# Kernel tuning notes

Measured on AMD Instinct MI355X. Metric: run time of the kernel, lower is better.

## Reference

```python
import jax, jax.numpy as jnp
import numpy as np

# ---- forest structure (static) ----
B = 32                      # number of trees in the batch
DEPTH = 12                  # topological levels per tree
LEVELS = [2 ** d for d in range(DEPTH)]           # nodes per level (root=level 0)
STARTS = np.concatenate([[0], np.cumsum(LEVELS)[:-1]]).astype(int)
NPG = int(sum(LEVELS))      # 4095 nodes per graph, node 0 = root
N = B * NPG                 # 131040 total nodes
VOCAB = 20000               # dataset.PAD_TOKEN_VALUE + 1
PAD = VOCAB - 1             # padding_idx
E = 256                     # embedding_dim (x_size)
H = 256                     # lstm_output_dim (h_size)
C = 104                     # num_classes (extra_non_linear=None)


def setup_inputs() -> dict:
    key = jax.random.key(0)
    ks = jax.random.split(key, 8)
    # random parent in the previous level for every non-root node (irregular fan-in)
    rng = np.random.RandomState(0)
    par = np.full(N, -1, dtype=np.int64)
    for g in range(B):
        off = g * NPG
        for d in range(1, DEPTH):
            nd = LEVELS[d]
            par[off + STARTS[d]: off + STARTS[d] + nd] = (
                off + STARTS[d - 1] + rng.randint(0, LEVELS[d - 1], size=nd))
    s = 0.05
    return {
        'x': jax.random.randint(ks[0], (N,), 0, VOCAB),
        'par': jnp.asarray(par),
        'emb': jax.random.normal(ks[1], (VOCAB, E), jnp.float32) * s,
        'W_iou': jax.random.normal(ks[2], (3 * H, E), jnp.float32) * s,
        'U_iou': jax.random.normal(ks[3], (3 * H, H), jnp.float32) * s,
        'b_iou': jnp.zeros((1, 3 * H), jnp.float32),
        'U_f_w': jax.random.normal(ks[4], (H, H), jnp.float32) * s,
        'U_f_b': jnp.zeros((H,), jnp.float32),
        'lin_w': jax.random.normal(ks[5], (C, H), jnp.float32) * s,
        'lin_b': jnp.zeros((C,), jnp.float32),
    }


def _forward(x, par, emb, W_iou, U_iou, b_iou, U_f_w, U_f_b, lin_w, lin_b):
    emb = emb.at[PAD].set(0.0)                 # padding_idx row is zero
    x_vec = emb[x]                             # [N, E]
    iou = x_vec @ W_iou.T                      # [N, 3H], W_iou has no bias
    h = jnp.zeros((N, H), x_vec.dtype)
    c = jnp.zeros((N, H), x_vec.dtype)
    offs = jnp.arange(B) * NPG
    # topological propagation: leaves (deepest level) -> root, per generation
    for d in range(DEPTH - 1, -1, -1):
        nd = LEVELS[d]
        nids = (offs[:, None] + STARTS[d] + jnp.arange(nd)).reshape(-1)  # [B*nd]
        iou_n = iou[nids]
        if d < DEPTH - 1:
            nc = LEVELS[d + 1]
            cids = (offs[:, None] + STARTS[d + 1] + jnp.arange(nc)).reshape(-1)
            h_ch = h[cids]                     # mailbox gather of child states
            c_ch = c[cids]
            p = par[cids]                      # global parent id per child
            seg = (p // NPG) * nd + (p % NPG - STARTS[d])  # parent slot in this level
            f = jax.nn.sigmoid(h_ch @ U_f_w.T + U_f_b)     # per-child forget gate
            h_tild = jax.ops.segment_sum(h_ch, seg, num_segments=B * nd)
            c_agg = jax.ops.segment_sum(f * c_ch, seg, num_segments=B * nd)
            iou_n = iou_n + h_tild @ U_iou.T
            c_n = c_agg
        else:
            c_n = jnp.zeros((B * nd, H), x_vec.dtype)
        iou_n = iou_n + b_iou
        i, o, u = jnp.split(iou_n, 3, axis=1)
        c_new = jax.nn.sigmoid(i) * jnp.tanh(u) + c_n
        h_new = jax.nn.sigmoid(o) * jnp.tanh(c_new)
        h = h.at[nids].set(h_new)
        c = c.at[nids].set(c_new)
    roots = h[offs]                            # graph.ndata['h'][0] per graph
    return roots @ lin_w.T + lin_b             # [B, num_classes]


def reference(x, par, emb, W_iou, U_iou, b_iou, U_f_w, U_f_b, lin_w, lin_b):
    return _forward(x, par, emb, W_iou, U_iou, b_iou, U_f_w, U_f_b, lin_w, lin_b)
```

## Files before the change

### kernel.cpp

```cpp
#include <hip/hip_runtime.h>
#include <hip/hip_bf16.h>


#define B_G     32
#define NPG     4095
#define NTOT    (B_G * NPG)
#define NCLS    104
#define VOCAB   20000
#define PAD_TOK 19999
#define KCAP    24
#define LB(d)   (32 * ((1 << (d)) - 1))

#define EMB_BLKS  2500
#define WUC_BLKS  1536
#define UFC_BLKS  256
#define PREP_BLKS 512
#define CONV_BLKS (EMB_BLKS + WUC_BLKS + UFC_BLKS + PREP_BLKS)

typedef unsigned short u16;
typedef unsigned int   u32;
typedef __attribute__((ext_vector_type(8))) short bfrag8;
typedef __attribute__((ext_vector_type(4))) float ffrag4;

__device__ __forceinline__ float bf2f(u16 v) {
    union { u32 u; float f; } x; x.u = ((u32)v) << 16; return x.f;
}
__device__ __forceinline__ u16 f2bf(float f) {
    union { __hip_bfloat16 h; u16 u; } c; c.h = __float2bfloat16(f); return c.u;
}
__device__ __forceinline__ float loadv(const void* b, int i, int isf32) {
    return isf32 ? ((const float*)b)[i] : bf2f(((const u16*)b)[i]);
}
__device__ __forceinline__ float sigf(float x) { return 1.f / (1.f + __expf(-x)); }

__global__ __launch_bounds__(384) void probe_kernel(
    const void* emb, const void* Wiou, const void* Uiou,
    const void* Ufw, const void* lw,
    const int* x32, const int* par32, int* flags)
{
    if (blockIdx.x != 0) return;
    const int w = threadIdx.x >> 6, lane = threadIdx.x & 63;
    const void* ptrs[5] = { emb, Wiou, Uiou, Ufw, lw };
    if (w < 5) {
        const u16* p = (const u16*)ptrs[w];
        int big = 0;
        #pragma unroll
        for (int k = 0; k < 2; ++k) {
            u32 e = (((u32)p[lane * 2 + k]) << 16 >> 23) & 0xFF;
            if (e >= 129) ++big;
        }
        unsigned long long m1 = __ballot(big >= 1);
        unsigned long long m2 = __ballot(big >= 2);
        int tot = __popcll(m1) + __popcll(m2);
        if (lane == 0) flags[w] = (tot >= 4) ? 1 : 0;
    } else if (w == 5) {
        int bad = (lane < 8) ? (x32[2 * lane + 1] != 0) : 0;
        unsigned long long mx = __ballot(bad != 0);
        if (lane == 0) {
            flags[5] = (mx == 0) ? 1 : 0;
            flags[6] = (par32[3] == 0 && par32[5] == 0) ? 1 : 0;
        }
    }
}

__global__ __launch_bounds__(256) void convert_kernel(
    const void* __restrict__ emb, u16* __restrict__ embb,
    const void* __restrict__ Wiou, const void* __restrict__ Uiou,
    u16* __restrict__ wuc,
    const void* __restrict__ Ufw, u16* __restrict__ ufc,
    const int* __restrict__ x, const int* __restrict__ par,
    int* __restrict__ tokLvl, int* __restrict__ cnt, int* __restrict__ bucket,
    const int* __restrict__ flags)
{
    const int b = blockIdx.x;
    if (b < EMB_BLKS) {
        int i8 = (b * 256 + (int)threadIdx.x) * 8;
        if (i8 >= VOCAB * 256) return;
        u16 v[8];
        if ((i8 >> 8) == PAD_TOK) {
            #pragma unroll
            for (int s = 0; s < 8; ++s) v[s] = 0;
        } else if (flags[0]) {
            const float* e = (const float*)emb + i8;
            float4 a = *(const float4*)e;
            float4 c = *(const float4*)(e + 4);
            v[0]=f2bf(a.x); v[1]=f2bf(a.y); v[2]=f2bf(a.z); v[3]=f2bf(a.w);
            v[4]=f2bf(c.x); v[5]=f2bf(c.y); v[6]=f2bf(c.z); v[7]=f2bf(c.w);
        } else {
            *(uint4*)v = *(const uint4*)((const u16*)emb + i8);
        }
        *(uint4*)(embb + i8) = *(uint4*)v;
    } else if (b < EMB_BLKS + WUC_BLKS) {
        int idx = (b - EMB_BLKS) * 256 + (int)threadIdx.x;
        if (idx >= 16 * 768 * 32) return;
        int c   = idx / 24576;
        int rem = idx - c * 24576;
        int out = rem >> 5;
        int kk  = rem & 31;
        int k   = c * 32 + kk;
        float v = (k < 256) ? loadv(Wiou, out * 256 + k, flags[1])
                            : loadv(Uiou, out * 256 + (k - 256), flags[2]);
        wuc[idx] = f2bf(v);
    } else if (b < EMB_BLKS + WUC_BLKS + UFC_BLKS) {
        int idx = (b - EMB_BLKS - WUC_BLKS) * 256 + (int)threadIdx.x;
        if (idx >= 8 * 256 * 32) return;
        int c   = idx >> 13;
        int rem = idx & 8191;
        int out = rem >> 5;
        int kk  = rem & 31;
        ufc[idx] = f2bf(loadv(Ufw, out * 256 + c * 32 + kk, flags[3]));
    } else {
        int gid = (b - EMB_BLKS - WUC_BLKS - UFC_BLKS) * 256 + (int)threadIdx.x;
        if (gid >= NTOT) return;
        int g     = (int)((u32)gid / NPG);
        int local = gid - g * NPG;
        int v  = local + 1;
        int d  = 31 - __clz(v);
        int j  = local - ((1 << d) - 1);
        int tok = flags[5] ? x[2 * gid] : x[gid];
        if (tok < 0 || tok >= VOCAB) tok = PAD_TOK;
        tokLvl[LB(d) + (g << d) + j] = tok;
        if (local > 0) {
            int p  = flags[6] ? par[2 * gid] : par[gid];
            p = max(0, min(p, NTOT - 1));
            int pg = (int)((u32)p / NPG);
            int pl = p - pg * NPG;
            int pd = d - 1;
            int ps = LB(pd) + (pg << pd) + (pl - ((1 << pd) - 1));
            ps = max(0, min(ps, 65503));
            int slot = atomicAdd(&cnt[ps], 1);
            if (slot < KCAP) bucket[(size_t)ps * KCAP + slot] = (g << d) + j;
        }
    }
}

__global__ __launch_bounds__(256, 3) void gemm1_kernel(
    const u16* __restrict__ hch, u16* cbuf,
    const u16* __restrict__ ufc, const void* __restrict__ ufb,
    const int* __restrict__ flags)
{
    __shared__ union {
        struct { u16 As[2][64][40]; u16 Bs[2][256][40]; } k;
        u16 tile[64][264];
    } sm;
    auto& tile = sm.tile;
    const int t = threadIdx.x;
    const int w = t >> 6, lane = t & 63, quad = lane >> 4, l15 = lane & 15;
    const int m0 = blockIdx.x * 64;
    const int f_uf = flags[3];

    ffrag4 acc[4][4];
    #pragma unroll
    for (int i = 0; i < 4; ++i)
        #pragma unroll
        for (int j = 0; j < 4; ++j) acc[i][j] = (ffrag4)0.f;

    const int arow = t >> 2, aseg = t & 3;

    *(uint4*)&sm.k.As[0][arow][aseg * 8] =
        *(const uint4*)(hch + (size_t)(m0 + arow) * 256 + aseg * 8);
    #pragma unroll
    for (int r16 = 0; r16 < 4; ++r16)
        *(uint4*)&sm.k.Bs[0][r16 * 64 + arow][aseg * 8] =
            *(const uint4*)(ufc + ((size_t)r16 * 64 + arow) * 32 + aseg * 8);
    __syncthreads();

    for (int c = 0; c < 8; ++c) {
        const int cur = c & 1, nxt = cur ^ 1;
        const bool more = (c + 1 < 8);
        uint4 ra, rb0, rb1, rb2, rb3;
        if (more) {
            const int cn = c + 1;
            ra  = *(const uint4*)(hch + (size_t)(m0 + arow) * 256 + cn * 32 + aseg * 8);
            rb0 = *(const uint4*)(ufc + ((size_t)cn * 256 +   0 + arow) * 32 + aseg * 8);
            rb1 = *(const uint4*)(ufc + ((size_t)cn * 256 +  64 + arow) * 32 + aseg * 8);
            rb2 = *(const uint4*)(ufc + ((size_t)cn * 256 + 128 + arow) * 32 + aseg * 8);
            rb3 = *(const uint4*)(ufc + ((size_t)cn * 256 + 192 + arow) * 32 + aseg * 8);
        }
        bfrag8 a[4], b[4];
        #pragma unroll
        for (int mt = 0; mt < 4; ++mt) a[mt] = *(bfrag8*)&sm.k.As[cur][mt * 16 + l15][quad * 8];
        #pragma unroll
        for (int nt = 0; nt < 4; ++nt) b[nt] = *(bfrag8*)&sm.k.Bs[cur][w * 64 + nt * 16 + l15][quad * 8];
        #pragma unroll
        for (int mt = 0; mt < 4; ++mt)
            #pragma unroll
            for (int nt = 0; nt < 4; ++nt)
                acc[mt][nt] = __builtin_amdgcn_mfma_f32_16x16x32_bf16(a[mt], b[nt], acc[mt][nt], 0, 0, 0);
        if (more) {
            *(uint4*)&sm.k.As[nxt][arow][aseg * 8] = ra;
            *(uint4*)&sm.k.Bs[nxt][  0 + arow][aseg * 8] = rb0;
            *(uint4*)&sm.k.Bs[nxt][ 64 + arow][aseg * 8] = rb1;
            *(uint4*)&sm.k.Bs[nxt][128 + arow][aseg * 8] = rb2;
            *(uint4*)&sm.k.Bs[nxt][192 + arow][aseg * 8] = rb3;
        }
        __syncthreads();
    }

    const int srow = t >> 2, sseg = t & 3;
    const size_t sgb = (size_t)(m0 + srow) * 256 + sseg * 64;
    #pragma unroll
    for (int k = 0; k < 8; ++k)
        *(uint4*)&tile[srow][sseg * 64 + k * 8] = *(const uint4*)(cbuf + sgb + k * 8);
    __syncthreads();

    #pragma unroll
    for (int nt = 0; nt < 4; ++nt) {
        int hu = w * 64 + nt * 16 + l15;
        float fb = loadv(ufb, hu, f_uf);
        #pragma unroll
        for (int mt = 0; mt < 4; ++mt) {
            #pragma unroll
            for (int r = 0; r < 4; ++r) {
                int row = mt * 16 + quad * 4 + r;
                float f = sigf(acc[mt][nt][r] + fb);
                tile[row][hu] = f2bf(f * bf2f(tile[row][hu]));
            }
        }
    }
    __syncthreads();
    #pragma unroll
    for (int k = 0; k < 8; ++k)
        *(uint4*)(cbuf + sgb + k * 8) = *(const uint4*)&tile[srow][sseg * 64 + k * 8];
}

__global__ __launch_bounds__(256) void agg_kernel(
    int NN, const u32* __restrict__ hch32, const u32* __restrict__ fcch32,
    const int* __restrict__ cnt_d, const int* __restrict__ bucket_d,
    u32* __restrict__ htild32, u32* __restrict__ cagg32)
{
    int pi  = blockIdx.x * 2 + (threadIdx.x >> 7);
    int col = threadIdx.x & 127;
    if (pi >= NN) return;
    int nc = min(cnt_d[pi], KCAP);
    float h0 = 0.f, h1 = 0.f, c0 = 0.f, c1 = 0.f;
    for (int ci = 0; ci < nc; ++ci) {
        int ch = bucket_d[(size_t)pi * KCAP + ci];
        u32 hv = hch32[(size_t)ch * 128 + col];
        u32 fv = fcch32[(size_t)ch * 128 + col];
        h0 += bf2f((u16)(hv & 0xffff)); h1 += bf2f((u16)(hv >> 16));
        c0 += bf2f((u16)(fv & 0xffff)); c1 += bf2f((u16)(fv >> 16));
    }
    htild32[(size_t)pi * 128 + col] = (u32)f2bf(h0) | ((u32)f2bf(h1) << 16);
    cagg32[(size_t)pi * 128 + col]  = (u32)f2bf(c0) | ((u32)f2bf(c1) << 16);
}

__global__ __launch_bounds__(256, 3) void gemm2_kernel(
    int nchunk, int NN,
    const int* __restrict__ tokLvl_d, const u16* __restrict__ embb,
    const u16* __restrict__ wuc, const void* __restrict__ biou,
    const u16* __restrict__ htild, const u16* __restrict__ cagg,
    u16* __restrict__ hdst, u16* __restrict__ cdst,
    const int* __restrict__ flags)
{
    __shared__ union {
        struct { u16 As[2][128][40]; u16 Bs[2][192][40]; } k;
        u16 tile[128][72];
    } sm;
    __shared__ int toks[128];
    auto& tile = sm.tile;
    const int t = threadIdx.x;
    const int w = t >> 6, lane = t & 63, quad = lane >> 4, l15 = lane & 15;
    const int m0 = blockIdx.x * 128;
    const int q  = blockIdx.y;
    const int f_b = flags[1];

    if (t < 128) toks[t] = tokLvl_d[m0 + t];
    __syncthreads();

    ffrag4 acc[8][3];
    #pragma unroll
    for (int i = 0; i < 8; ++i)
        #pragma unroll
        for (int j = 0; j < 3; ++j) acc[i][j] = (ffrag4)0.f;

    const int arow = t >> 1, ac0 = (t & 1) * 16;
    const int brow = t >> 2, bseg = t & 3;

    {
        const u16* e = embb + (size_t)toks[arow] * 256 + ac0;
        *(uint4*)&sm.k.As[0][arow][ac0]     = *(const uint4*)e;
        *(uint4*)&sm.k.As[0][arow][ac0 + 8] = *(const uint4*)(e + 8);
        #pragma unroll
        for (int g = 0; g < 3; ++g)
            *(uint4*)&sm.k.Bs[0][g * 64 + brow][bseg * 8] =
                *(const uint4*)(wuc + ((size_t)g * 256 + q * 64 + brow) * 32 + bseg * 8);
    }
    __syncthreads();

    for (int c = 0; c < nchunk; ++c) {
        const int cur = c & 1, nxt = cur ^ 1;
        const bool more = (c + 1 < nchunk);
        uint4 ra0, ra1, rb0, rb1, rb2;
        if (more) {
            const int cn = c + 1;
            const u16* asrc = (cn < 8)
                ? embb  + (size_t)toks[arow] * 256 + cn * 32 + ac0
                : htild + (size_t)(m0 + arow) * 256 + (cn - 8) * 32 + ac0;
            ra0 = *(const uint4*)asrc;
            ra1 = *(const uint4*)(asrc + 8);
            const u16* bsrc = wuc + ((size_t)cn * 768 + q * 64 + brow) * 32 + bseg * 8;
            rb0 = *(const uint4*)bsrc;
            rb1 = *(const uint4*)(bsrc + (size_t)256 * 32);
            rb2 = *(const uint4*)(bsrc + (size_t)512 * 32);
        }
        bfrag8 a[8], b[3];
        #pragma unroll
        for (int mt = 0; mt < 8; ++mt) a[mt] = *(bfrag8*)&sm.k.As[cur][mt * 16 + l15][quad * 8];
        #pragma unroll
        for (int g = 0; g < 3; ++g) b[g] = *(bfrag8*)&sm.k.Bs[cur][g * 64 + w * 16 + l15][quad * 8];
        #pragma unroll
        for (int mt = 0; mt < 8; ++mt)
            #pragma unroll
            for (int g = 0; g < 3; ++g)
                acc[mt][g] = __builtin_amdgcn_mfma_f32_16x16x32_bf16(a[mt], b[g], acc[mt][g], 0, 0, 0);
        if (more) {
            *(uint4*)&sm.k.As[nxt][arow][ac0]     = ra0;
            *(uint4*)&sm.k.As[nxt][arow][ac0 + 8] = ra1;
            *(uint4*)&sm.k.Bs[nxt][  0 + brow][bseg * 8] = rb0;
            *(uint4*)&sm.k.Bs[nxt][ 64 + brow][bseg * 8] = rb1;
            *(uint4*)&sm.k.Bs[nxt][128 + brow][bseg * 8] = rb2;
        }
        __syncthreads();
    }

    const int hu  = q * 64 + w * 16 + l15;
    const int huL = w * 16 + l15;
    const float bi = loadv(biou, hu,       f_b);
    const float bo = loadv(biou, 256 + hu, f_b);
    const float bu = loadv(biou, 512 + hu, f_b);

    const int srow = t >> 1, sseg = t & 1;
    const size_t sgbase = (size_t)(m0 + srow) * 256 + q * 64 + sseg * 32;
    const bool svalid = (m0 + srow) < NN;

    if (cagg) {
        if (svalid) {
            #pragma unroll
            for (int k = 0; k < 4; ++k)
                *(uint4*)&tile[srow][sseg * 32 + k * 8] =
                    *(const uint4*)(cagg + sgbase + k * 8);
        }
    }
    __syncthreads();

    u16 cnv[8][4];
    #pragma unroll
    for (int mt = 0; mt < 8; ++mt) {
        #pragma unroll
        for (int r = 0; r < 4; ++r) {
            int row = mt * 16 + quad * 4 + r;
            float cg = cagg ? bf2f(tile[row][huL]) : 0.f;
            float iv = acc[mt][0][r] + bi;
            float ov = acc[mt][1][r] + bo;
            float uv = acc[mt][2][r] + bu;
            float cn = sigf(iv) * tanhf(uv) + cg;
            float hn = sigf(ov) * tanhf(cn);
            cnv[mt][r] = f2bf(cn);
            tile[row][huL] = f2bf(hn);
        }
    }
    __syncthreads();
    if (svalid) {
        #pragma unroll
        for (int k = 0; k < 4; ++k)
            *(uint4*)(hdst + sgbase + k * 8) = *(const uint4*)&tile[srow][sseg * 32 + k * 8];
    }
    __syncthreads();
    #pragma unroll
    for (int mt = 0; mt < 8; ++mt)
        #pragma unroll
        for (int r = 0; r < 4; ++r)
            tile[mt * 16 + quad * 4 + r][huL] = cnv[mt][r];
    __syncthreads();
    if (svalid) {
        #pragma unroll
        for (int k = 0; k < 4; ++k)
            *(uint4*)(cdst + sgbase + k * 8) = *(const uint4*)&tile[srow][sseg * 32 + k * 8];
    }
}

__global__ __launch_bounds__(1024, 1) void tail_kernel(
    const int* __restrict__ tokLvl, const u16* __restrict__ embb,
    const u16* __restrict__ wuc, const void* __restrict__ biou,
    const u16* __restrict__ ufc, const void* __restrict__ ufb,
    const u16* __restrict__ hB, const u16* __restrict__ cB,
    const int* __restrict__ cnt, const int* __restrict__ bucket,
    const void* __restrict__ lw, const void* __restrict__ lb,
    float* __restrict__ out, const int* __restrict__ flags)
{
    __shared__ u16 hs[64][264];
    __shared__ u16 cs[64][264];
    __shared__ u16 hts[32][264];
    __shared__ u16 cts[32][264];
    __shared__ float lred[8][NCLS];
    __shared__ int cntS[64];
    __shared__ int toksS[64];
    __shared__ int bucketS[64][KCAP];
    const int t = threadIdx.x;
    const int g = blockIdx.x;
    const int w = t >> 6;
    const int lane = t & 63, quad = lane >> 4, l15 = lane & 15;
    const int f_uf = flags[3], f_b = flags[1], f_lw = flags[4];
    const int hu = w * 16 + l15;

    const float fbv = loadv(ufb, hu, f_uf);
    const float biv = loadv(biou, hu,       f_b);
    const float bov = loadv(biou, 256 + hu, f_b);
    const float buv = loadv(biou, 512 + hu, f_b);

    #pragma unroll 1
    for (int i = t; i < 64 * 32; i += 1024) {
        int j = i >> 5, seg = i & 31;
        size_t off = (((size_t)((g << 6) + j)) << 8) + seg * 8;
        *(uint4*)&hs[j][seg * 8] = *(const uint4*)(hB + off);
        *(uint4*)&cs[j][seg * 8] = *(const uint4*)(cB + off);
    }
    #pragma unroll 1
    for (int d5 = 5; d5 >= 0; --d5) {
        const int np5  = 1 << d5;
        const int sb5  = 64 - (2 << d5);
        const int lvb5 = LB(d5) + (g << d5);
        #pragma unroll 1
        for (int i = t; i < np5 * (KCAP + 1); i += 1024) {
            int pi = i / (KCAP + 1), f = i - pi * (KCAP + 1);
            if (f == 0) {
                cntS[sb5 + pi]  = cnt[lvb5 + pi];
                toksS[sb5 + pi] = tokLvl[lvb5 + pi];
            } else {
                bucketS[sb5 + pi][f - 1] = bucket[(size_t)(lvb5 + pi) * KCAP + f - 1];
            }
        }
    }
    __syncthreads();

    #pragma unroll 1
    for (int d = 5; d >= 0; --d) {
        const int ncr = 1 << (d + 1);
        const int np  = 1 << d;
        const int sb  = 64 - (2 << d);

        {
            ffrag4 facc[4];
            #pragma unroll
            for (int i = 0; i < 4; ++i) facc[i] = (ffrag4)0.f;
            #pragma unroll 4
            for (int c = 0; c < 8; ++c) {
                bfrag8 a[4];
                #pragma unroll
                for (int mt = 0; mt < 4; ++mt)
                    a[mt] = *(const bfrag8*)&hs[mt * 16 + l15][c * 32 + quad * 8];
                bfrag8 b = *(const bfrag8*)(ufc + ((size_t)c * 256 + w * 16 + l15) * 32 + quad * 8);
                #pragma unroll
                for (int mt = 0; mt < 4; ++mt)
                    facc[mt] = __builtin_amdgcn_mfma_f32_16x16x32_bf16(a[mt], b, facc[mt], 0, 0, 0);
            }
            #pragma unroll
            for (int mt = 0; mt < 4; ++mt) {
                #pragma unroll
                for (int r = 0; r < 4; ++r) {
                    int j = mt * 16 + quad * 4 + r;
                    if (j < ncr) {
                        float f = sigf(facc[mt][r] + fbv);
                        cs[j][hu] = f2bf(f * bf2f(cs[j][hu]));
                    }
                }
            }
        }

        {
            const int pr = lane >> 3;
            const int colb = (w * 8 + (lane & 7)) * 2;
            #pragma unroll 1
            for (int pi = pr; pi < np; pi += 8) {
                int nc = min(cntS[sb + pi], KCAP);
                float h0 = 0.f, h1 = 0.f, c0 = 0.f, c1 = 0.f;
                #pragma unroll 1
                for (int ci = 0; ci < nc; ++ci) {
                    int j = bucketS[sb + pi][ci] & (ncr - 1);
                    u32 hv = *(const u32*)&hs[j][colb];
                    u32 cv = *(const u32*)&cs[j][colb];
                    h0 += bf2f((u16)(hv & 0xffff)); h1 += bf2f((u16)(hv >> 16));
                    c0 += bf2f((u16)(cv & 0xffff)); c1 += bf2f((u16)(cv >> 16));
                }
                *(u32*)&hts[pi][colb] = (u32)f2bf(h0) | ((u32)f2bf(h1) << 16);
                *(u32*)&cts[pi][colb] = (u32)f2bf(c0) | ((u32)f2bf(c1) << 16);
            }
        }
        __syncthreads();

        {
            int tok0 = toksS[sb + min(l15, np - 1)];
            int tok1 = toksS[sb + min(16 + l15, np - 1)];
            const u16* wb = wuc + ((size_t)w * 16 + l15) * 32 + quad * 8;
            ffrag4 acc[2][3];
            #pragma unroll
            for (int i = 0; i < 2; ++i)
                #pragma unroll
                for (int j = 0; j < 3; ++j) acc[i][j] = (ffrag4)0.f;
            #pragma unroll 4
            for (int c = 0; c < 8; ++c) {
                bfrag8 a0 = *(const bfrag8*)(embb + (size_t)tok0 * 256 + c * 32 + quad * 8);
                bfrag8 a1 = *(const bfrag8*)(embb + (size_t)tok1 * 256 + c * 32 + quad * 8);
                #pragma unroll
                for (int g3 = 0; g3 < 3; ++g3) {
                    bfrag8 b = *(const bfrag8*)(wb + ((size_t)c * 768 + g3 * 256) * 32);
                    acc[0][g3] = __builtin_amdgcn_mfma_f32_16x16x32_bf16(a0, b, acc[0][g3], 0, 0, 0);
                    acc[1][g3] = __builtin_amdgcn_mfma_f32_16x16x32_bf16(a1, b, acc[1][g3], 0, 0, 0);
                }
            }
            #pragma unroll 4
            for (int c8 = 0; c8 < 8; ++c8) {
                bfrag8 a0 = *(const bfrag8*)&hts[l15][c8 * 32 + quad * 8];
                bfrag8 a1 = *(const bfrag8*)&hts[16 + l15][c8 * 32 + quad * 8];
                #pragma unroll
                for (int g3 = 0; g3 < 3; ++g3) {
                    bfrag8 b = *(const bfrag8*)(wb + ((size_t)(c8 + 8) * 768 + g3 * 256) * 32);
                    acc[0][g3] = __builtin_amdgcn_mfma_f32_16x16x32_bf16(a0, b, acc[0][g3], 0, 0, 0);
                    acc[1][g3] = __builtin_amdgcn_mfma_f32_16x16x32_bf16(a1, b, acc[1][g3], 0, 0, 0);
                }
            }
            #pragma unroll
            for (int mt = 0; mt < 2; ++mt) {
                #pragma unroll
                for (int r = 0; r < 4; ++r) {
                    int p = mt * 16 + quad * 4 + r;
                    if (p < np) {
                        float iv = acc[mt][0][r] + biv;
                        float ov = acc[mt][1][r] + bov;
                        float uv = acc[mt][2][r] + buv;
                        float cn = sigf(iv) * tanhf(uv) + bf2f(cts[p][hu]);
                        float hn = sigf(ov) * tanhf(cn);
                        hs[p][hu] = f2bf(hn);
                        cs[p][hu] = f2bf(cn);
                    }
                }
            }
        }
        __syncthreads();
    }

    {
        const int o  = t & 127;
        const int ks = t >> 7;
        if (o < NCLS) {
            float acc = 0.f;
            #pragma unroll 8
            for (int k = ks * 32; k < ks * 32 + 32; ++k)
                acc += loadv(lw, o * 256 + k, f_lw) * bf2f(hs[0][k]);
            lred[ks][o] = acc;
        }
        __syncthreads();
        if (t < NCLS) {
            float s = 0.f;
            #pragma unroll
            for (int i = 0; i < 8; ++i) s += lred[i][t];
            out[(size_t)g * NCLS + t] = s + loadv(lb, t, f_lw);
        }
    }
}

__global__ void fill_kernel(float* out, int n, float v) {
    int i = blockIdx.x * 256 + threadIdx.x;
    if (i < n) out[i] = v;
}

extern "C" void kernel_launch(void* const* d_in, const int* in_sizes, int n_in,
                              void* d_out, int out_size, void* d_ws, size_t ws_size,
                              hipStream_t stream)
{
    float* out = (float*)d_out;

    static const int exp_sizes[10] = {131040, 131040, 5120000, 196608, 196608,
                                      768, 65536, 256, 26624, 104};
    bool shapes_ok = (n_in == 10) && (out_size == B_G * NCLS);
    for (int i = 0; i < 10 && shapes_ok; ++i)
        if (in_sizes[i] != exp_sizes[i]) shapes_ok = false;
    if (!shapes_ok) {
        fill_kernel<<<(out_size + 255) / 256, 256, 0, stream>>>(out, out_size, 2.0f);
        return;
    }

    const int* x     = (const int*)d_in[0];
    const int* par   = (const int*)d_in[1];
    const void* emb  = d_in[2];
    const void* Wiou = d_in[3];
    const void* Uiou = d_in[4];
    const void* biou = d_in[5];
    const void* Ufw  = d_in[6];
    const void* Ufb  = d_in[7];
    const void* lw   = d_in[8];
    const void* lb   = d_in[9];

    char* W = (char*)d_ws;
    u16* hA     = (u16*)(W + 0);
    u16* hB     = (u16*)(W + 33554432);
    u16* cA     = (u16*)(W + 50331648);
    u16* cB     = (u16*)(W + 83886080);
    u16* htild  = (u16*)(W + 100663296);
    u16* cagg   = (u16*)(W + 117440512);
    u16* WUc    = (u16*)(W + 134217728);
    u16* Ufc    = (u16*)(W + 135004160);
    int* tokLvl = (int*)(W + 135135232);
    int* cnt    = (int*)(W + 135659520);
    int* bucket = (int*)(W + 135921664);
    u16* embb   = (u16*)(W + 142213120);
    int* flags  = (int*)(W + 152453120);
    const size_t NEED = 152453184;
    if (ws_size < NEED) {
        fill_kernel<<<(out_size + 255) / 256, 256, 0, stream>>>(out, out_size, 1.0f);
        return;
    }

    hipMemsetAsync(cnt, 0, 65536 * sizeof(int), stream);
    probe_kernel<<<1, 384, 0, stream>>>(emb, Wiou, Uiou, Ufw, lw, x, par, flags);
    convert_kernel<<<CONV_BLKS, 256, 0, stream>>>(
        emb, embb, Wiou, Uiou, WUc, Ufw, Ufc,
        x, par, tokLvl, cnt, bucket, flags);

    gemm2_kernel<<<dim3(512, 4), 256, 0, stream>>>(
        8, 65536, tokLvl + LB(11), embb, WUc, biou,
        nullptr, nullptr, hA, cA, flags);

    for (int d = 10; d >= 6; --d) {
        const int cl = d + 1;
        const int NC = B_G << cl;
        const int NN = B_G << d;
        const u16* hch = (cl & 1) ? hA : hB;
        u16*       cch = (cl & 1) ? cA : cB;
        u16* hdst = (d & 1) ? hA : hB;
        u16* cdst = (d & 1) ? cA : cB;
        gemm1_kernel<<<NC / 64, 256, 0, stream>>>(hch, cch, Ufc, Ufb, flags);
        agg_kernel<<<(NN + 1) / 2, 256, 0, stream>>>(
            NN, (const u32*)hch, (const u32*)cch,
            cnt + LB(d), bucket + (size_t)LB(d) * KCAP,
            (u32*)htild, (u32*)cagg);
        gemm2_kernel<<<dim3((NN + 127) / 128, 4), 256, 0, stream>>>(
            16, NN, tokLvl + LB(d), embb, WUc, biou,
            htild, cagg, hdst, cdst, flags);
    }

    tail_kernel<<<B_G, 1024, 0, stream>>>(
        tokLvl, embb, WUc, biou, Ufc, Ufb,
        hB, cB, cnt, bucket, lw, lb, out, flags);
}
```

Baseline: 596.0 us.

## Load GEMM weight tiles directly into LDS with XOR-swizzled layout

Weight tiles for the two GEMM kernels are now copied from global memory straight into shared memory with global_load_lds, so they no longer pass through registers. To make this work without padding, the shared B tiles drop from a 40-wide to a 32-wide row, and the packed weight layout is XOR-swizzled at conversion time to avoid bank conflicts. Every consumer of wuc/ufc, including the tail kernel that reads those weights straight from global memory, now uses the matching swizzled index. The goals are lower register pressure and fewer VGPR round trips, at the cost of depending on the direct-to-LDS load path behaving correctly with the existing barriers.

```diff
diff --git a/kernel.cpp b/kernel.cpp
--- a/kernel.cpp
+++ b/kernel.cpp
@@ -32,6 +32,12 @@
     return isf32 ? ((const float*)b)[i] : bf2f(((const u16*)b)[i]);
 }
 __device__ __forceinline__ float sigf(float x) { return 1.f / (1.f + __expf(-x)); }
+
+__device__ __forceinline__ void gll16(const u16* g, u16* l) {
+    __builtin_amdgcn_global_load_lds(
+        (const __attribute__((address_space(1))) u32*)g,
+        (__attribute__((address_space(3))) u32*)l, 16, 0, 0);
+}
 
 __global__ __launch_bounds__(384) void probe_kernel(
     const void* emb, const void* Wiou, const void* Uiou,
@@ -97,7 +103,8 @@
         int rem = idx - c * 24576;
         int out = rem >> 5;
         int kk  = rem & 31;
-        int k   = c * 32 + kk;
+        int kks = (((kk >> 3) ^ ((out >> 1) & 3)) << 3) | (kk & 7);
+        int k   = c * 32 + kks;
         float v = (k < 256) ? loadv(Wiou, out * 256 + k, flags[1])
                             : loadv(Uiou, out * 256 + (k - 256), flags[2]);
         wuc[idx] = f2bf(v);
@@ -108,7 +115,8 @@
         int rem = idx & 8191;
         int out = rem >> 5;
         int kk  = rem & 31;
-        ufc[idx] = f2bf(loadv(Ufw, out * 256 + c * 32 + kk, flags[3]));
+        int kks = (((kk >> 3) ^ ((out >> 1) & 3)) << 3) | (kk & 7);
+        ufc[idx] = f2bf(loadv(Ufw, out * 256 + c * 32 + kks, flags[3]));
     } else {
         int gid = (b - EMB_BLKS - WUC_BLKS - UFC_BLKS) * 256 + (int)threadIdx.x;
         if (gid >= NTOT) return;
@@ -140,12 +148,13 @@
     const int* __restrict__ flags)
 {
     __shared__ union {
-        struct { u16 As[2][64][40]; u16 Bs[2][256][40]; } k;
+        struct { u16 As[2][64][40]; u16 Bs[2][256][32]; } k;
         u16 tile[64][264];
     } sm;
     auto& tile = sm.tile;
     const int t = threadIdx.x;
     const int w = t >> 6, lane = t & 63, quad = lane >> 4, l15 = lane & 15;
+    const int squad = quad ^ ((l15 >> 1) & 3);
     const int m0 = blockIdx.x * 64;
     const int f_uf = flags[3];
 
@@ -161,39 +170,34 @@
         *(const uint4*)(hch + (size_t)(m0 + arow) * 256 + aseg * 8);
     #pragma unroll
     for (int r16 = 0; r16 < 4; ++r16)
-        *(uint4*)&sm.k.Bs[0][r16 * 64 + arow][aseg * 8] =
-            *(const uint4*)(ufc + ((size_t)r16 * 64 + arow) * 32 + aseg * 8);
+        gll16(ufc + ((size_t)r16 * 64 + arow) * 32 + aseg * 8,
+              &sm.k.Bs[0][r16 * 64 + arow][aseg * 8]);
     __syncthreads();
 
     for (int c = 0; c < 8; ++c) {
         const int cur = c & 1, nxt = cur ^ 1;
         const bool more = (c + 1 < 8);
-        uint4 ra, rb0, rb1, rb2, rb3;
+        uint4 ra;
         if (more) {
             const int cn = c + 1;
-            ra  = *(const uint4*)(hch + (size_t)(m0 + arow) * 256 + cn * 32 + aseg * 8);
-            rb0 = *(const uint4*)(ufc + ((size_t)cn * 256 +   0 + arow) * 32 + aseg * 8);
-            rb1 = *(const uint4*)(ufc + ((size_t)cn * 256 +  64 + arow) * 32 + aseg * 8);
-            rb2 = *(const uint4*)(ufc + ((size_t)cn * 256 + 128 + arow) * 32 + aseg * 8);
-            rb3 = *(const uint4*)(ufc + ((size_t)cn * 256 + 192 + arow) * 32 + aseg * 8);
+            ra = *(const uint4*)(hch + (size_t)(m0 + arow) * 256 + cn * 32 + aseg * 8);
+            #pragma unroll
+            for (int r16 = 0; r16 < 4; ++r16)
+                gll16(ufc + ((size_t)cn * 256 + r16 * 64 + arow) * 32 + aseg * 8,
+                      &sm.k.Bs[nxt][r16 * 64 + arow][aseg * 8]);
         }
         bfrag8 a[4], b[4];
         #pragma unroll
         for (int mt = 0; mt < 4; ++mt) a[mt] = *(bfrag8*)&sm.k.As[cur][mt * 16 + l15][quad * 8];
         #pragma unroll
-        for (int nt = 0; nt < 4; ++nt) b[nt] = *(bfrag8*)&sm.k.Bs[cur][w * 64 + nt * 16 + l15][quad * 8];
+        for (int nt = 0; nt < 4; ++nt) b[nt] = *(bfrag8*)&sm.k.Bs[cur][w * 64 + nt * 16 + l15][squad * 8];
         #pragma unroll
         for (int mt = 0; mt < 4; ++mt)
             #pragma unroll
             for (int nt = 0; nt < 4; ++nt)
                 acc[mt][nt] = __builtin_amdgcn_mfma_f32_16x16x32_bf16(a[mt], b[nt], acc[mt][nt], 0, 0, 0);
-        if (more) {
+        if (more)
             *(uint4*)&sm.k.As[nxt][arow][aseg * 8] = ra;
-            *(uint4*)&sm.k.Bs[nxt][  0 + arow][aseg * 8] = rb0;
-            *(uint4*)&sm.k.Bs[nxt][ 64 + arow][aseg * 8] = rb1;
-            *(uint4*)&sm.k.Bs[nxt][128 + arow][aseg * 8] = rb2;
-            *(uint4*)&sm.k.Bs[nxt][192 + arow][aseg * 8] = rb3;
-        }
         __syncthreads();
     }
 
@@ -254,13 +258,14 @@
     const int* __restrict__ flags)
 {
     __shared__ union {
-        struct { u16 As[2][128][40]; u16 Bs[2][192][40]; } k;
+        struct { u16 As[2][128][40]; u16 Bs[2][192][32]; } k;
         u16 tile[128][72];
     } sm;
     __shared__ int toks[128];
     auto& tile = sm.tile;
     const int t = threadIdx.x;
     const int w = t >> 6, lane = t & 63, quad = lane >> 4, l15 = lane & 15;
+    const int squad = quad ^ ((l15 >> 1) & 3);
     const int m0 = blockIdx.x * 128;
     const int q  = blockIdx.y;
     const int f_b = flags[1];
@@ -283,15 +288,15 @@
         *(uint4*)&sm.k.As[0][arow][ac0 + 8] = *(const uint4*)(e + 8);
         #pragma unroll
         for (int g = 0; g < 3; ++g)
-            *(uint4*)&sm.k.Bs[0][g * 64 + brow][bseg * 8] =
-                *(const uint4*)(wuc + ((size_t)g * 256 + q * 64 + brow) * 32 + bseg * 8);
+            gll16(wuc + ((size_t)g * 256 + q * 64 + brow) * 32 + bseg * 8,
+                  &sm.k.Bs[0][g * 64 + brow][bseg * 8]);
     }
     __syncthreads();
 
     for (int c = 0; c < nchunk; ++c) {
         const int cur = c & 1, nxt = cur ^ 1;
         const bool more = (c + 1 < nchunk);
-        uint4 ra0, ra1, rb0, rb1, rb2;
+        uint4 ra0, ra1;
         if (more) {
             const int cn = c + 1;
             const u16* asrc = (cn < 8)
@@ -299,16 +304,16 @@
                 : htild + (size_t)(m0 + arow) * 256 + (cn - 8) * 32 + ac0;
             ra0 = *(const uint4*)asrc;
             ra1 = *(const uint4*)(asrc + 8);
-            const u16* bsrc = wuc + ((size_t)cn * 768 + q * 64 + brow) * 32 + bseg * 8;
-            rb0 = *(const uint4*)bsrc;
-            rb1 = *(const uint4*)(bsrc + (size_t)256 * 32);
-            rb2 = *(const uint4*)(bsrc + (size_t)512 * 32);
+            #pragma unroll
+            for (int g = 0; g < 3; ++g)
+                gll16(wuc + ((size_t)cn * 768 + g * 256 + q * 64 + brow) * 32 + bseg * 8,
+                      &sm.k.Bs[nxt][g * 64 + brow][bseg * 8]);
         }
         bfrag8 a[8], b[3];
         #pragma unroll
         for (int mt = 0; mt < 8; ++mt) a[mt] = *(bfrag8*)&sm.k.As[cur][mt * 16 + l15][quad * 8];
         #pragma unroll
-        for (int g = 0; g < 3; ++g) b[g] = *(bfrag8*)&sm.k.Bs[cur][g * 64 + w * 16 + l15][quad * 8];
+        for (int g = 0; g < 3; ++g) b[g] = *(bfrag8*)&sm.k.Bs[cur][g * 64 + w * 16 + l15][squad * 8];
         #pragma unroll
         for (int mt = 0; mt < 8; ++mt)
             #pragma unroll
@@ -317,9 +322,6 @@
         if (more) {
             *(uint4*)&sm.k.As[nxt][arow][ac0]     = ra0;
             *(uint4*)&sm.k.As[nxt][arow][ac0 + 8] = ra1;
-            *(uint4*)&sm.k.Bs[nxt][  0 + brow][bseg * 8] = rb0;
-            *(uint4*)&sm.k.Bs[nxt][ 64 + brow][bseg * 8] = rb1;
-            *(uint4*)&sm.k.Bs[nxt][128 + brow][bseg * 8] = rb2;
         }
         __syncthreads();
     }
@@ -401,6 +403,7 @@
     const int g = blockIdx.x;
     const int w = t >> 6;
     const int lane = t & 63, quad = lane >> 4, l15 = lane & 15;
+    const int squad = quad ^ ((l15 >> 1) & 3);
     const int f_uf = flags[3], f_b = flags[1], f_lw = flags[4];
     const int hu = w * 16 + l15;
 
@@ -450,7 +453,7 @@
                 #pragma unroll
                 for (int mt = 0; mt < 4; ++mt)
                     a[mt] = *(const bfrag8*)&hs[mt * 16 + l15][c * 32 + quad * 8];
-                bfrag8 b = *(const bfrag8*)(ufc + ((size_t)c * 256 + w * 16 + l15) * 32 + quad * 8);
+                bfrag8 b = *(const bfrag8*)(ufc + ((size_t)c * 256 + w * 16 + l15) * 32 + squad * 8);
                 #pragma unroll
                 for (int mt = 0; mt < 4; ++mt)
                     facc[mt] = __builtin_amdgcn_mfma_f32_16x16x32_bf16(a[mt], b, facc[mt], 0, 0, 0);
@@ -492,7 +495,7 @@
         {
             int tok0 = toksS[sb + min(l15, np - 1)];
             int tok1 = toksS[sb + min(16 + l15, np - 1)];
-            const u16* wb = wuc + ((size_t)w * 16 + l15) * 32 + quad * 8;
+            const u16* wb = wuc + ((size_t)w * 16 + l15) * 32 + squad * 8;
             ffrag4 acc[2][3];
             #pragma unroll
             for (int i = 0; i < 2; ++i)
```

New measurement: 580.0 us. 2.7% less time.
